# Kernel optimization log

Measured on AMD Instinct MI355X. Metric: run time of the kernel, lower is better.

## Reference

```python
import jax, jax.numpy as jnp
import numpy as np

B, T, I, H, L, O = 256, 256, 64, 2048, 4, 1

def setup_inputs() -> dict:
    key = jax.random.key(0)
    ks = jax.random.split(key, 8)
    # layer 0: input_size -> hidden (xavier-uniform-like scale)
    W_ih0 = jax.random.normal(ks[0], (H, I), jnp.float32) * (1.0 / np.sqrt(I))
    b_ih0 = jnp.zeros((H,), jnp.float32)
    # layers 1..L-1: hidden -> hidden, stacked
    W_ih_rest = jax.random.normal(ks[1], (L - 1, H, H), jnp.float32) * (1.0 / np.sqrt(H))
    b_ih_rest = jnp.zeros((L - 1, H), jnp.float32)
    # recurrent weights for all layers (orthogonal init approximated by scaled normal)
    W_hh = jax.random.normal(ks[2], (L, H, H), jnp.float32) * (1.0 / np.sqrt(H))
    # final fc
    W_fc = jax.random.normal(ks[3], (O, H), jnp.float32) * (1.0 / np.sqrt(H))
    b_fc = jnp.zeros((O,), jnp.float32)
    x = jax.random.normal(ks[4], (B, T, I), jnp.float32)
    return {"x": x, "W_ih0": W_ih0, "b_ih0": b_ih0, "W_ih_rest": W_ih_rest,
            "b_ih_rest": b_ih_rest, "W_hh": W_hh, "W_fc": W_fc, "b_fc": b_fc}

def reference(x, W_ih0, b_ih0, W_ih_rest, b_ih_rest, W_hh, W_fc, b_fc):
    # h_t^l = tanh(W_ih^l @ inp + b_ih^l + W_hh^l @ h_{t-1}^l); dropout_rate=0 (identity)
    h0 = jnp.zeros((L, B, H), x.dtype)
    xs = jnp.swapaxes(x, 0, 1)  # [T, B, I]

    def step(h, x_t):
        inp = x_t
        new_h = []
        for l in range(L):
            if l == 0:
                pre = inp @ W_ih0.T + b_ih0 + h[l] @ W_hh[l].T
            else:
                pre = inp @ W_ih_rest[l - 1].T + b_ih_rest[l - 1] + h[l] @ W_hh[l].T
            hl = jnp.tanh(pre)
            new_h.append(hl)
            inp = hl
        return jnp.stack(new_h, 0), None

    h_final, _ = jax.lax.scan(step, h0, xs)
    return h_final[-1] @ W_fc.T + b_fc  # [B, O]
```

## Files before the change

### kernel.cpp

```cpp
#include <hip/hip_runtime.h>
#include <hip/hip_bf16.h>


typedef unsigned short u16;
typedef __attribute__((ext_vector_type(8))) short short8;
typedef __attribute__((ext_vector_type(4))) float f32x4;

#define T_N 256
#define B_N 256
#define I_N 64
#define H_N 2048
#define L_N 4

static constexpr size_t S0_ELE = 2048ull * 2112ull;
static constexpr size_t SL_ELE = 2048ull * 4096ull;
static constexpr size_t WT_ELEMS = S0_ELE + 3ull * SL_ELE;
static constexpr size_t XS_ELEMS = 256ull * 256ull * 64ull;
static constexpr size_t HSLOT    = 256ull * 2048ull;
static constexpr size_t H_ELEMS  = 2ull * 4ull * HSLOT;

__device__ __forceinline__ u16 f2bf(float v) {
  __hip_bfloat16 b = __float2bfloat16(v);
  u16 u; __builtin_memcpy(&u, &b, 2); return u;
}
__device__ __forceinline__ float bf2f(u16 u) {
  __hip_bfloat16 b; __builtin_memcpy(&b, &u, 2);
  return __bfloat162float(b);
}

__global__ void prep_w(const float* __restrict__ W_ih0, const float* __restrict__ W_ih_rest,
                       const float* __restrict__ W_hh,
                       u16* __restrict__ wt_hi, u16* __restrict__ wt_lo) {
  const unsigned TOT = (unsigned)WT_ELEMS;
  for (unsigned i = blockIdx.x * 256u + threadIdx.x; i < TOT; i += gridDim.x * 256u) {
    int l, K, Kin; unsigned r;
    if (i < (unsigned)S0_ELE) { l = 0; r = i; K = 2112; Kin = 64; }
    else {
      unsigned j = i - (unsigned)S0_ELE;
      l = 1 + (int)(j / (unsigned)SL_ELE);
      r = j % (unsigned)SL_ELE; K = 4096; Kin = 2048;
    }
    unsigned n = r / (unsigned)K, k = r % (unsigned)K;
    float v;
    if ((int)k < Kin)
      v = (l == 0) ? W_ih0[(size_t)n * 64 + k]
                   : W_ih_rest[(((size_t)(l - 1)) * 2048 + n) * 2048 + k];
    else
      v = W_hh[(((size_t)l) * 2048 + n) * 2048 + (k - (unsigned)Kin)];
    u16 hi = f2bf(v);
    wt_hi[i] = hi;
    wt_lo[i] = f2bf(v - bf2f(hi));
  }
}

__global__ void prep_x(const float* __restrict__ x, u16* __restrict__ xs_hi, u16* __restrict__ xs_lo) {
  for (unsigned i = blockIdx.x * 256u + threadIdx.x; i < (unsigned)XS_ELEMS; i += gridDim.x * 256u) {
    float v = x[i];
    u16 hi = f2bf(v);
    xs_hi[i] = hi;
    xs_lo[i] = f2bf(v - bf2f(hi));
  }
}

__launch_bounds__(256)
__global__ void phase_k(const u16* __restrict__ wt_hi, const u16* __restrict__ wt_lo,
                        const u16* __restrict__ xs_hi, const u16* __restrict__ xs_lo,
                        u16* __restrict__ h_hi, u16* __restrict__ h_lo,
                        const float* __restrict__ b_ih0, const float* __restrict__ b_ih_rest,
                        int s) {
  int bid = blockIdx.x;
  int xcd = bid & 7, slot = bid >> 3;
  int tm = slot & 3;
  int tn = (xcd << 1) | ((slot >> 2) & 1);
  int l  = slot >> 3;
  int t  = s - l;
  if (t < 0 || t >= T_N) return;

  const int Kl  = (l == 0) ? 2112 : 4096;
  const int Kin = (l == 0) ? 64 : 2048;
  const size_t woff = (l == 0) ? 0ull : (S0_ELE + (size_t)(l - 1) * SL_ELE);
  const u16* wl_hi = wt_hi + woff;
  const u16* wl_lo = wt_lo + woff;

  const size_t ho_out  = ((size_t)((t & 1) * 4 + l)) * HSLOT;
  const size_t ho_self = ((size_t)(((t - 1) & 1) * 4 + l)) * HSLOT;
  const int lprev = (l > 0) ? (l - 1) : 0;
  const size_t ho_prevL = ((size_t)((t & 1) * 4 + lprev)) * HSLOT;

  __shared__ __align__(16) u16 Ahi[64 * 64];
  __shared__ __align__(16) u16 Alo[64 * 64];
  __shared__ __align__(16) u16 Bhi[128 * 64];
  __shared__ __align__(16) u16 Blo[128 * 64];

  const int tid = threadIdx.x;
  const int lane = tid & 63;
  const int l15 = lane & 15, g16 = lane >> 4;
  const int wid = tid >> 6;
  const int wave_m = (wid & 1) * 32, wave_n = (wid >> 1) * 64;

  f32x4 acc[2][4];
#pragma unroll
  for (int mi = 0; mi < 2; ++mi)
#pragma unroll
    for (int ni = 0; ni < 4; ++ni)
      acc[mi][ni] = (f32x4){0.f, 0.f, 0.f, 0.f};

  short8 sa_h[2], sa_l[2], sb_h[4], sb_l[4];

  auto load_chunk = [&](int kc) {
#pragma unroll
    for (int it = 0; it < 2; ++it) {
      int G = it * 256 + tid;
      int r = G >> 3, gl = G & 7;
      int kg = (kc << 6) + (gl << 3);
      int b = tm * 64 + r;
      const u16 *ph, *pl; size_t o;
      if (kg < Kin) {
        if (l == 0) { o = ((size_t)b * T_N + t) * I_N + kg; ph = xs_hi; pl = xs_lo; }
        else        { o = ho_prevL + (size_t)b * H_N + kg;  ph = h_hi;  pl = h_lo; }
      } else        { o = ho_self + (size_t)b * H_N + (kg - Kin); ph = h_hi; pl = h_lo; }
      sa_h[it] = *(const short8*)(ph + o);
      sa_l[it] = *(const short8*)(pl + o);
    }
#pragma unroll
    for (int it = 0; it < 4; ++it) {
      int G = it * 256 + tid;
      int r = G >> 3, gl = G & 7;
      int kg = (kc << 6) + (gl << 3);
      size_t o = (size_t)(tn * 128 + r) * Kl + kg;
      sb_h[it] = *(const short8*)(wl_hi + o);
      sb_l[it] = *(const short8*)(wl_lo + o);
    }
  };
  auto write_chunk = [&]() {
#pragma unroll
    for (int it = 0; it < 2; ++it) {
      int G = it * 256 + tid;
      int r = G >> 3, gl = G & 7;
      int idx = r * 64 + (gl ^ (r & 7)) * 8;
      *(short8*)&Ahi[idx] = sa_h[it];
      *(short8*)&Alo[idx] = sa_l[it];
    }
#pragma unroll
    for (int it = 0; it < 4; ++it) {
      int G = it * 256 + tid;
      int r = G >> 3, gl = G & 7;
      int idx = r * 64 + (gl ^ (r & 7)) * 8;
      *(short8*)&Bhi[idx] = sb_h[it];
      *(short8*)&Blo[idx] = sb_l[it];
    }
  };

  const int nchunks = Kl >> 6;
  load_chunk(0);
  for (int kc = 0; kc < nchunks; ++kc) {
    __syncthreads();
    write_chunk();
    __syncthreads();
    if (kc + 1 < nchunks) load_chunk(kc + 1);

#pragma unroll
    for (int ks = 0; ks < 2; ++ks) {
      const int glb = (ks << 2) + g16;
      short8 ah[2], al[2], bh[4], bl[4];
#pragma unroll
      for (int mi = 0; mi < 2; ++mi) {
        int r = wave_m + mi * 16 + l15;
        int idx = r * 64 + (glb ^ (r & 7)) * 8;
        ah[mi] = *(const short8*)&Ahi[idx];
        al[mi] = *(const short8*)&Alo[idx];
      }
#pragma unroll
      for (int ni = 0; ni < 4; ++ni) {
        int r = wave_n + ni * 16 + l15;
        int idx = r * 64 + (glb ^ (r & 7)) * 8;
        bh[ni] = *(const short8*)&Bhi[idx];
        bl[ni] = *(const short8*)&Blo[idx];
      }
#pragma unroll
      for (int mi = 0; mi < 2; ++mi)
#pragma unroll
        for (int ni = 0; ni < 4; ++ni) {
          acc[mi][ni] = __builtin_amdgcn_mfma_f32_16x16x32_bf16(ah[mi], bh[ni], acc[mi][ni], 0, 0, 0);
          acc[mi][ni] = __builtin_amdgcn_mfma_f32_16x16x32_bf16(ah[mi], bl[ni], acc[mi][ni], 0, 0, 0);
          acc[mi][ni] = __builtin_amdgcn_mfma_f32_16x16x32_bf16(al[mi], bh[ni], acc[mi][ni], 0, 0, 0);
        }
    }
  }

  const float* bias = (l == 0) ? b_ih0 : (b_ih_rest + (size_t)(l - 1) * H_N);
#pragma unroll
  for (int mi = 0; mi < 2; ++mi)
#pragma unroll
    for (int ni = 0; ni < 4; ++ni)
#pragma unroll
      for (int rg = 0; rg < 4; ++rg) {
        int bg = tm * 64 + wave_m + mi * 16 + g16 * 4 + rg;
        int ng = tn * 128 + wave_n + ni * 16 + l15;
        float v = acc[mi][ni][rg] + bias[ng];
        v = tanhf(v);
        u16 hi = f2bf(v);
        size_t o = ho_out + (size_t)bg * H_N + ng;
        h_hi[o] = hi;
        h_lo[o] = f2bf(v - bf2f(hi));
      }
}

__global__ void fc_k(const u16* __restrict__ h_hi, const u16* __restrict__ h_lo,
                     const float* __restrict__ W_fc, const float* __restrict__ b_fc,
                     float* __restrict__ out) {
  int b = blockIdx.x, tid = threadIdx.x;
  size_t base = ((size_t)(((T_N - 1) & 1) * 4 + 3)) * HSLOT + (size_t)b * H_N;
  float s = 0.f;
  for (int j = tid; j < H_N; j += 256)
    s += (bf2f(h_hi[base + j]) + bf2f(h_lo[base + j])) * W_fc[j];
  __shared__ float red[256];
  red[tid] = s; __syncthreads();
  for (int w = 128; w > 0; w >>= 1) {
    if (tid < w) red[tid] += red[tid + w];
    __syncthreads();
  }
  if (tid == 0) out[b] = red[0] + b_fc[0];
}

extern "C" void kernel_launch(void* const* d_in, const int* in_sizes, int n_in,
                              void* d_out, int out_size, void* d_ws, size_t ws_size,
                              hipStream_t stream) {
  const float* x         = (const float*)d_in[0];
  const float* W_ih0     = (const float*)d_in[1];
  const float* b_ih0     = (const float*)d_in[2];
  const float* W_ih_rest = (const float*)d_in[3];
  const float* b_ih_rest = (const float*)d_in[4];
  const float* W_hh      = (const float*)d_in[5];
  const float* W_fc      = (const float*)d_in[6];
  const float* b_fc      = (const float*)d_in[7];
  float* out = (float*)d_out;

  char* p = (char*)d_ws;
  auto carve = [&](size_t bytes) {
    char* q = p; p += (bytes + 255) & ~(size_t)255; return q;
  };
  u16* wt_hi = (u16*)carve(WT_ELEMS * 2);
  u16* wt_lo = (u16*)carve(WT_ELEMS * 2);
  u16* xs_hi = (u16*)carve(XS_ELEMS * 2);
  u16* xs_lo = (u16*)carve(XS_ELEMS * 2);
  u16* h_hi  = (u16*)carve(H_ELEMS * 2);
  u16* h_lo  = (u16*)carve(H_ELEMS * 2);

  hipMemsetAsync(h_hi, 0, H_ELEMS * 2 * 2, stream);
  prep_w<<<4096, 256, 0, stream>>>(W_ih0, W_ih_rest, W_hh, wt_hi, wt_lo);
  prep_x<<<2048, 256, 0, stream>>>(x, xs_hi, xs_lo);

  for (int s = 0; s < T_N + L_N - 1; ++s)
    phase_k<<<256, 256, 0, stream>>>(wt_hi, wt_lo, xs_hi, xs_lo, h_hi, h_lo,
                                     b_ih0, b_ih_rest, s);

  fc_k<<<256, 256, 0, stream>>>(h_hi, h_lo, W_fc, b_fc, out);
}
```

Before: 19.25 ms.

## Use direct global-to-LDS loads with double buffering and smaller N tiles

```diff
diff --git a/kernel.cpp b/kernel.cpp
--- a/kernel.cpp
+++ b/kernel.cpp
@@ -7,7 +7,6 @@
 typedef __attribute__((ext_vector_type(4))) float f32x4;
 
 #define T_N 256
-#define B_N 256
 #define I_N 64
 #define H_N 2048
 #define L_N 4
@@ -26,6 +25,12 @@
 __device__ __forceinline__ float bf2f(u16 u) {
   __hip_bfloat16 b; __builtin_memcpy(&b, &u, 2);
   return __bfloat162float(b);
+}
+
+__device__ __forceinline__ void gl2lds16(const u16* g, u16* l) {
+  __builtin_amdgcn_global_load_lds(
+      (const __attribute__((address_space(1))) unsigned int*)g,
+      (__attribute__((address_space(3))) unsigned int*)l, 16, 0, 0);
 }
 
 __global__ void prep_w(const float* __restrict__ W_ih0, const float* __restrict__ W_ih_rest,
@@ -62,7 +67,7 @@
   }
 }
 
-__launch_bounds__(256)
+__launch_bounds__(256, 2)
 __global__ void phase_k(const u16* __restrict__ wt_hi, const u16* __restrict__ wt_lo,
                         const u16* __restrict__ xs_hi, const u16* __restrict__ xs_lo,
                         u16* __restrict__ h_hi, u16* __restrict__ h_lo,
@@ -70,14 +75,14 @@
                         int s) {
   int bid = blockIdx.x;
   int xcd = bid & 7, slot = bid >> 3;
-  int tm = slot & 3;
-  int tn = (xcd << 1) | ((slot >> 2) & 1);
-  int l  = slot >> 3;
-  int t  = s - l;
+  int tm  = slot & 3;
+  int tnl = (slot >> 2) & 3;
+  int l   = slot >> 4;
+  int tn  = xcd * 4 + tnl;
+  int t   = s - l;
   if (t < 0 || t >= T_N) return;
 
   const int Kl  = (l == 0) ? 2112 : 4096;
-  const int Kin = (l == 0) ? 64 : 2048;
   const size_t woff = (l == 0) ? 0ull : (S0_ELE + (size_t)(l - 1) * SL_ELE);
   const u16* wl_hi = wt_hi + woff;
   const u16* wl_lo = wt_lo + woff;
@@ -87,100 +92,87 @@
   const int lprev = (l > 0) ? (l - 1) : 0;
   const size_t ho_prevL = ((size_t)((t & 1) * 4 + lprev)) * HSLOT;
 
-  __shared__ __align__(16) u16 Ahi[64 * 64];
-  __shared__ __align__(16) u16 Alo[64 * 64];
-  __shared__ __align__(16) u16 Bhi[128 * 64];
-  __shared__ __align__(16) u16 Blo[128 * 64];
+  __shared__ __align__(16) u16 Ahi[2][64 * 64];
+  __shared__ __align__(16) u16 Alo[2][64 * 64];
+  __shared__ __align__(16) u16 Bhi[2][64 * 64];
+  __shared__ __align__(16) u16 Blo[2][64 * 64];
 
   const int tid = threadIdx.x;
   const int lane = tid & 63;
   const int l15 = lane & 15, g16 = lane >> 4;
   const int wid = tid >> 6;
-  const int wave_m = (wid & 1) * 32, wave_n = (wid >> 1) * 64;
-
-  f32x4 acc[2][4];
+  const int wave_m = (wid & 1) * 32, wave_n = (wid >> 1) * 32;
+
+  f32x4 acc[2][2];
 #pragma unroll
   for (int mi = 0; mi < 2; ++mi)
 #pragma unroll
-    for (int ni = 0; ni < 4; ++ni)
+    for (int ni = 0; ni < 2; ++ni)
       acc[mi][ni] = (f32x4){0.f, 0.f, 0.f, 0.f};
 
-  short8 sa_h[2], sa_l[2], sb_h[4], sb_l[4];
-
-  auto load_chunk = [&](int kc) {
+  const int selfc0 = (l == 0) ? 1 : 32;
+  const int kin    = (l == 0) ? 64 : 2048;
+
+  auto issue_chunk = [&](int kc, int buf) {
 #pragma unroll
     for (int it = 0; it < 2; ++it) {
       int G = it * 256 + tid;
       int r = G >> 3, gl = G & 7;
-      int kg = (kc << 6) + (gl << 3);
+      int kg = (kc << 6) + ((gl ^ (r & 7)) << 3);
       int b = tm * 64 + r;
       const u16 *ph, *pl; size_t o;
-      if (kg < Kin) {
+      if (kc < selfc0) {
         if (l == 0) { o = ((size_t)b * T_N + t) * I_N + kg; ph = xs_hi; pl = xs_lo; }
         else        { o = ho_prevL + (size_t)b * H_N + kg;  ph = h_hi;  pl = h_lo; }
-      } else        { o = ho_self + (size_t)b * H_N + (kg - Kin); ph = h_hi; pl = h_lo; }
-      sa_h[it] = *(const short8*)(ph + o);
-      sa_l[it] = *(const short8*)(pl + o);
-    }
-#pragma unroll
-    for (int it = 0; it < 4; ++it) {
-      int G = it * 256 + tid;
-      int r = G >> 3, gl = G & 7;
-      int kg = (kc << 6) + (gl << 3);
-      size_t o = (size_t)(tn * 128 + r) * Kl + kg;
-      sb_h[it] = *(const short8*)(wl_hi + o);
-      sb_l[it] = *(const short8*)(wl_lo + o);
-    }
-  };
-  auto write_chunk = [&]() {
+      } else {
+        o = ho_self + (size_t)b * H_N + (kg - kin); ph = h_hi; pl = h_lo;
+      }
+      u16* dh = &Ahi[buf][(it * 256 + wid * 64) * 8];
+      u16* dl = &Alo[buf][(it * 256 + wid * 64) * 8];
+      gl2lds16(ph + o, dh);
+      gl2lds16(pl + o, dl);
+    }
 #pragma unroll
     for (int it = 0; it < 2; ++it) {
       int G = it * 256 + tid;
       int r = G >> 3, gl = G & 7;
-      int idx = r * 64 + (gl ^ (r & 7)) * 8;
-      *(short8*)&Ahi[idx] = sa_h[it];
-      *(short8*)&Alo[idx] = sa_l[it];
-    }
-#pragma unroll
-    for (int it = 0; it < 4; ++it) {
-      int G = it * 256 + tid;
-      int r = G >> 3, gl = G & 7;
-      int idx = r * 64 + (gl ^ (r & 7)) * 8;
-      *(short8*)&Bhi[idx] = sb_h[it];
-      *(short8*)&Blo[idx] = sb_l[it];
+      size_t o = (size_t)(tn * 64 + r) * Kl + (kc << 6) + ((gl ^ (r & 7)) << 3);
+      u16* dh = &Bhi[buf][(it * 256 + wid * 64) * 8];
+      u16* dl = &Blo[buf][(it * 256 + wid * 64) * 8];
+      gl2lds16(wl_hi + o, dh);
+      gl2lds16(wl_lo + o, dl);
     }
   };
 
   const int nchunks = Kl >> 6;
-  load_chunk(0);
+  issue_chunk(0, 0);
   for (int kc = 0; kc < nchunks; ++kc) {
+    const int cur = kc & 1;
     __syncthreads();
-    write_chunk();
-    __syncthreads();
-    if (kc + 1 < nchunks) load_chunk(kc + 1);
+    if (kc + 1 < nchunks) issue_chunk(kc + 1, cur ^ 1);
 
 #pragma unroll
     for (int ks = 0; ks < 2; ++ks) {
       const int glb = (ks << 2) + g16;
-      short8 ah[2], al[2], bh[4], bl[4];
+      short8 ah[2], al[2], bh[2], bl[2];
 #pragma unroll
       for (int mi = 0; mi < 2; ++mi) {
         int r = wave_m + mi * 16 + l15;
-        int idx = r * 64 + (glb ^ (r & 7)) * 8;
-        ah[mi] = *(const short8*)&Ahi[idx];
-        al[mi] = *(const short8*)&Alo[idx];
-      }
-#pragma unroll
-      for (int ni = 0; ni < 4; ++ni) {
+        int idx = r * 64 + ((glb ^ (r & 7)) << 3);
+        ah[mi] = *(const short8*)&Ahi[cur][idx];
+        al[mi] = *(const short8*)&Alo[cur][idx];
+      }
+#pragma unroll
+      for (int ni = 0; ni < 2; ++ni) {
         int r = wave_n + ni * 16 + l15;
-        int idx = r * 64 + (glb ^ (r & 7)) * 8;
-        bh[ni] = *(const short8*)&Bhi[idx];
-        bl[ni] = *(const short8*)&Blo[idx];
+        int idx = r * 64 + ((glb ^ (r & 7)) << 3);
+        bh[ni] = *(const short8*)&Bhi[cur][idx];
+        bl[ni] = *(const short8*)&Blo[cur][idx];
       }
 #pragma unroll
       for (int mi = 0; mi < 2; ++mi)
 #pragma unroll
-        for (int ni = 0; ni < 4; ++ni) {
+        for (int ni = 0; ni < 2; ++ni) {
           acc[mi][ni] = __builtin_amdgcn_mfma_f32_16x16x32_bf16(ah[mi], bh[ni], acc[mi][ni], 0, 0, 0);
           acc[mi][ni] = __builtin_amdgcn_mfma_f32_16x16x32_bf16(ah[mi], bl[ni], acc[mi][ni], 0, 0, 0);
           acc[mi][ni] = __builtin_amdgcn_mfma_f32_16x16x32_bf16(al[mi], bh[ni], acc[mi][ni], 0, 0, 0);
@@ -192,11 +184,11 @@
 #pragma unroll
   for (int mi = 0; mi < 2; ++mi)
 #pragma unroll
-    for (int ni = 0; ni < 4; ++ni)
+    for (int ni = 0; ni < 2; ++ni)
 #pragma unroll
       for (int rg = 0; rg < 4; ++rg) {
         int bg = tm * 64 + wave_m + mi * 16 + g16 * 4 + rg;
-        int ng = tn * 128 + wave_n + ni * 16 + l15;
+        int ng = tn * 64 + wave_n + ni * 16 + l15;
         float v = acc[mi][ni][rg] + bias[ng];
         v = tanhf(v);
         u16 hi = f2bf(v);
@@ -252,7 +244,7 @@
   prep_x<<<2048, 256, 0, stream>>>(x, xs_hi, xs_lo);
 
   for (int s = 0; s < T_N + L_N - 1; ++s)
-    phase_k<<<256, 256, 0, stream>>>(wt_hi, wt_lo, xs_hi, xs_lo, h_hi, h_lo,
+    phase_k<<<512, 256, 0, stream>>>(wt_hi, wt_lo, xs_hi, xs_lo, h_hi, h_lo,
                                      b_ih0, b_ih_rest, s);
 
   fc_k<<<256, 256, 0, stream>>>(h_hi, h_lo, W_fc, b_fc, out);
```

New measurement: 16.59 ms. -13.9%, faster.
